# Kernel optimization log

Hardware: AMD Instinct MI355X
Metric: run time of the kernel (lower is better)

Reference implementation:

```python
import jax, jax.numpy as jnp
import numpy as np

NEG_INF = -1e30  # mask value used by QANet's apply_mask


def setup_inputs() -> dict:
    key = jax.random.key(0)
    ks = jax.random.split(key, 6)
    B, C, Q, H = 64, 1024, 128, 512
    return {
        "x_context": jax.random.normal(ks[0], (B, C, H), dtype=jnp.float32),
        "x_query": jax.random.normal(ks[1], (B, Q, H), dtype=jnp.float32),
        "context_mask": jnp.ones((B, C), dtype=jnp.float32),
        "query_mask": jnp.ones((B, Q), dtype=jnp.float32),
        "W0": jax.random.normal(ks[2], (H,), dtype=jnp.float32) * 0.05,
        "W1": jax.random.normal(ks[3], (H,), dtype=jnp.float32) * 0.05,
        "W2": jax.random.normal(ks[4], (H,), dtype=jnp.float32) * 0.05,
        "bias": jnp.zeros((1,), dtype=jnp.float32),
    }


def reference(x_context, x_query, context_mask, query_mask, W0, W1, W2, bias):
    # Trilinear similarity S[b,c,q] = q.W0 + c.W1 + (q*W2).c + bias
    # (original computes [B,Q,C] then transposes; we build [B,C,Q] directly)
    sub0 = jnp.einsum('bqh,h->bq', x_query, W0)          # [B,Q]
    sub1 = jnp.einsum('bch,h->bc', x_context, W1)        # [B,C]
    sub2 = jnp.einsum('bch,bqh->bcq', x_context, x_query * W2)  # [B,C,Q]
    S = sub2 + sub1[:, :, None] + sub0[:, None, :] + bias  # [B,C,Q]

    mq = query_mask[:, None, :]    # [B,1,Q]
    mc = context_mask[:, :, None]  # [B,C,1]

    # context-to-query: softmax over query axis, masked by query_mask
    S_ = jax.nn.softmax(S + (1.0 - mq) * NEG_INF, axis=-1)  # [B,C,Q]
    c2q = jnp.einsum('bcq,bqh->bch', S_, x_query)           # [B,C,H]

    # query-to-context: softmax over context axis, masked by context_mask
    S_c = jax.nn.softmax(S + (1.0 - mc) * NEG_INF, axis=1)  # [B,C,Q]
    S_T = jnp.swapaxes(S_c, 1, 2)                            # [B,Q,C]
    # (S_ @ S_T) @ x_context, associated as S_ @ (S_T @ x_context)
    tmp = jnp.einsum('bqc,bch->bqh', S_T, x_context)        # [B,Q,H]
    q2c = jnp.einsum('bcq,bqh->bch', S_, tmp)               # [B,C,H]
    return c2q, q2c
```

## Files before the change

kernel.cpp:

```cpp
#include <hip/hip_runtime.h>

#define BB 64
#define CC 1024
#define QQ 128
#define HH 512

typedef short bf16x8 __attribute__((ext_vector_type(8)));
typedef float f32x4 __attribute__((ext_vector_type(4)));

#define GLD16(g, l)                                                            \
    __builtin_amdgcn_global_load_lds(                                          \
        (const __attribute__((address_space(1))) unsigned int*)(g),            \
        (__attribute__((address_space(3))) unsigned int*)(l), 16, 0, 0)

__device__ __forceinline__ unsigned short f2bf(float f) {
    unsigned u = __float_as_uint(f);
    u += 0x7FFF + ((u >> 16) & 1);
    return (unsigned short)(u >> 16);
}
__device__ __forceinline__ unsigned pk2(float lo, float hi) {
    return (unsigned)f2bf(lo) | ((unsigned)f2bf(hi) << 16);
}

__global__ __launch_bounds__(256) void k_sub0(const float* __restrict__ xq,
                                              const float* __restrict__ w0,
                                              float* __restrict__ sub0,
                                              float* __restrict__ colsum) {
    if (blockIdx.x < 32) colsum[blockIdx.x * 256 + threadIdx.x] = 0.0f;
    int wave = threadIdx.x >> 6;
    int lane = threadIdx.x & 63;
    int row  = blockIdx.x * 4 + wave;
    const float* p = xq + (size_t)row * HH + lane * 8;
    float4 a0 = *(const float4*)(p);
    float4 a1 = *(const float4*)(p + 4);
    float4 b0 = *(const float4*)(w0 + lane * 8);
    float4 b1 = *(const float4*)(w0 + lane * 8 + 4);
    float s = a0.x*b0.x + a0.y*b0.y + a0.z*b0.z + a0.w*b0.w
            + a1.x*b1.x + a1.y*b1.y + a1.z*b1.z + a1.w*b1.w;
    #pragma unroll
    for (int off = 32; off; off >>= 1) s += __shfl_xor(s, off);
    if (lane == 0) sub0[row] = s;
}

__global__ __launch_bounds__(256) void k_prep(const float* __restrict__ xq,
                                              const float* __restrict__ w2,
                                              const float* __restrict__ qmask,
                                              unsigned short* __restrict__ xqw2b,
                                              unsigned short* __restrict__ xqmT) {
    int b  = blockIdx.y;
    int ht = blockIdx.x * 128;
    int tid = threadIdx.x;
    __shared__ __align__(16) unsigned short sT[128][132];

    {
        int q  = tid >> 1;
        int hh = (tid & 1) * 64;
        float qm = qmask[b * QQ + q];
        const float* xp = xq + ((size_t)b * QQ + q) * HH + ht + hh;
        unsigned short* wr = xqw2b + ((size_t)b * QQ + q) * HH + ht + hh;
        #pragma unroll
        for (int i = 0; i < 16; i++) {
            float4 v = *(const float4*)(xp + i * 4);
            float4 w = *(const float4*)(w2 + ht + hh + i * 4);
            uint2 pw; pw.x = pk2(v.x * w.x, v.y * w.y);
                      pw.y = pk2(v.z * w.z, v.w * w.w);
            *(uint2*)(wr + i * 4) = pw;
            uint2 pm; pm.x = pk2(v.x * qm, v.y * qm);
                      pm.y = pk2(v.z * qm, v.w * qm);
            *(uint2*)(&sT[q][hh + i * 4]) = pm;
        }
    }
    __syncthreads();
    {
        int h  = tid >> 1;
        int qh = (tid & 1) * 64;
        unsigned short* orow = xqmT + ((size_t)b * HH + ht + h) * QQ + qh;
        #pragma unroll
        for (int i = 0; i < 8; i++) {
            uint4 o;
            o.x = (unsigned)sT[qh + i*8 + 0][h] | ((unsigned)sT[qh + i*8 + 1][h] << 16);
            o.y = (unsigned)sT[qh + i*8 + 2][h] | ((unsigned)sT[qh + i*8 + 3][h] << 16);
            o.z = (unsigned)sT[qh + i*8 + 4][h] | ((unsigned)sT[qh + i*8 + 5][h] << 16);
            o.w = (unsigned)sT[qh + i*8 + 6][h] | ((unsigned)sT[qh + i*8 + 7][h] << 16);
            *(uint4*)(orow + i * 8) = o;
        }
    }
}

__global__ __launch_bounds__(256) void k_scores(
    const float* __restrict__ xc, const unsigned short* __restrict__ xqw2b,
    const float* __restrict__ w1, const float* __restrict__ cmask,
    const float* __restrict__ qmask, const float* __restrict__ bias,
    const float* __restrict__ sub0, unsigned short* __restrict__ Ebf,
    float* __restrict__ rowsum, float* __restrict__ colsum) {
    int b  = blockIdx.y;
    int c0 = blockIdx.x * 64;
    int tid  = threadIdx.x;
    int lane = tid & 63, wave = tid >> 6;
    int quad = lane >> 4, lcol = lane & 15;
    int wrow = (wave >> 1) * 32, wcol = (wave & 1) * 64;

    __shared__ __align__(16) unsigned short sA[2][64][32];
    __shared__ __align__(16) unsigned short sB[2][128][32];
    __shared__ float sW1[512];
    __shared__ float sSub1[64];
    __shared__ float sS0[128], sQm[128], sCm[64];
    __shared__ float sRowP[2][64], sColP[2][128];

    sW1[tid] = w1[tid]; sW1[tid + 256] = w1[tid + 256];
    if (tid < 128) {
        sS0[tid] = sub0[b * QQ + tid] + bias[0];
        sQm[tid] = qmask[b * QQ + tid];
    }
    if (tid < 64) sCm[tid] = cmask[b * CC + c0 + tid];

    f32x4 acc[2][4];
    #pragma unroll
    for (int i = 0; i < 2; i++)
        #pragma unroll
        for (int j = 0; j < 4; j++) acc[i][j] = (f32x4)0.0f;
    float s1 = 0.0f;

    int arow = tid >> 2, akh = (tid & 3) * 8;
    const float* gbase = xc + ((size_t)(b * CC + c0 + arow)) * HH + akh;

    __syncthreads();

    {
        float4 v0 = *(const float4*)(gbase);
        float4 v1 = *(const float4*)(gbase + 4);
        const float* wp = sW1 + akh;
        s1 += v0.x*wp[0] + v0.y*wp[1] + v0.z*wp[2] + v0.w*wp[3]
            + v1.x*wp[4] + v1.y*wp[5] + v1.z*wp[6] + v1.w*wp[7];
        uint4 p;
        p.x = pk2(v0.x, v0.y); p.y = pk2(v0.z, v0.w);
        p.z = pk2(v1.x, v1.y); p.w = pk2(v1.z, v1.w);
        *(uint4*)&sA[0][arow][akh] = p;
    }
    #pragma unroll
    for (int j = 0; j < 2; j++) {
        int chunk = wave * 2 + j;
        int row = chunk * 16 + (lane >> 2);
        GLD16(xqw2b + ((size_t)b * QQ + row) * HH + (lane & 3) * 8,
              (unsigned short*)sB[0] + chunk * 512);
    }
    __syncthreads();

    for (int t = 0; t < 16; ++t) {
        int cur = t & 1, alt = cur ^ 1;
        bool pf = (t < 15);
        int kn = (t + 1) * 32;
        float4 v0, v1;
        if (pf) {
            const float* gp = gbase + kn;
            v0 = *(const float4*)(gp);
            v1 = *(const float4*)(gp + 4);
            #pragma unroll
            for (int j = 0; j < 2; j++) {
                int chunk = wave * 2 + j;
                int row = chunk * 16 + (lane >> 2);
                GLD16(xqw2b + ((size_t)b * QQ + row) * HH + kn + (lane & 3) * 8,
                      (unsigned short*)sB[alt] + chunk * 512);
            }
        }
        bf16x8 af[2];
        #pragma unroll
        for (int mi = 0; mi < 2; mi++)
            af[mi] = *(const bf16x8*)&sA[cur][wrow + mi * 16 + lcol][quad * 8];
        #pragma unroll
        for (int ni = 0; ni < 4; ni++) {
            bf16x8 bfr = *(const bf16x8*)&sB[cur][wcol + ni * 16 + lcol][quad * 8];
            #pragma unroll
            for (int mi = 0; mi < 2; mi++)
                acc[mi][ni] = __builtin_amdgcn_mfma_f32_16x16x32_bf16(
                    af[mi], bfr, acc[mi][ni], 0, 0, 0);
        }
        if (pf) {
            const float* wp = sW1 + kn + akh;
            s1 += v0.x*wp[0] + v0.y*wp[1] + v0.z*wp[2] + v0.w*wp[3]
                + v1.x*wp[4] + v1.y*wp[5] + v1.z*wp[6] + v1.w*wp[7];
            uint4 p;
            p.x = pk2(v0.x, v0.y); p.y = pk2(v0.z, v0.w);
            p.z = pk2(v1.x, v1.y); p.w = pk2(v1.z, v1.w);
            *(uint4*)&sA[alt][arow][akh] = p;
        }
        __syncthreads();
    }

    s1 += __shfl_xor(s1, 1);
    s1 += __shfl_xor(s1, 2);
    if ((tid & 3) == 0) sSub1[arow] = s1;
    __syncthreads();

    float rsp[2][4];
    float csp[4] = {0.f, 0.f, 0.f, 0.f};
    #pragma unroll
    for (int mi = 0; mi < 2; mi++)
        #pragma unroll
        for (int r = 0; r < 4; r++) rsp[mi][r] = 0.f;

    #pragma unroll
    for (int mi = 0; mi < 2; mi++) {
        #pragma unroll
        for (int ni = 0; ni < 4; ni++) {
            int col = wcol + ni * 16 + lcol;
            float qm = sQm[col], s0 = sS0[col];
            #pragma unroll
            for (int r = 0; r < 4; r++) {
                int row = wrow + mi * 16 + quad * 4 + r;
                float e = __expf(acc[mi][ni][r] + sSub1[row] + s0);
                acc[mi][ni][r] = e;
                rsp[mi][r] += e * qm;
                csp[ni] += e * sCm[row];
            }
        }
    }
    #pragma unroll
    for (int mi = 0; mi < 2; mi++)
        #pragma unroll
        for (int r = 0; r < 4; r++) {
            float v = rsp[mi][r];
            v += __shfl_xor(v, 1); v += __shfl_xor(v, 2);
            v += __shfl_xor(v, 4); v += __shfl_xor(v, 8);
            if (lcol == 0) sRowP[wave & 1][wrow + mi * 16 + quad * 4 + r] = v;
        }
    #pragma unroll
    for (int ni = 0; ni < 4; ni++) {
        float v = csp[ni];
        v += __shfl_xor(v, 16); v += __shfl_xor(v, 32);
        if (quad == 0) sColP[wave >> 1][wcol + ni * 16 + lcol] = v;
    }
    #pragma unroll
    for (int mi = 0; mi < 2; mi++)
        #pragma unroll
        for (int ni = 0; ni < 4; ni++) {
            int col = wcol + ni * 16 + lcol;
            #pragma unroll
            for (int r = 0; r < 4; r++) {
                int row = wrow + mi * 16 + quad * 4 + r;
                Ebf[((size_t)(b * CC + c0 + row)) * QQ + col] = f2bf(acc[mi][ni][r]);
            }
        }
    __syncthreads();
    if (tid < 64)
        rowsum[(size_t)b * CC + c0 + tid] = sRowP[0][tid] + sRowP[1][tid];
    if (tid < 128)
        atomicAdd(&colsum[b * QQ + tid], sColP[0][tid] + sColP[1][tid]);
}

__global__ __launch_bounds__(256) void k_tmp(
    const unsigned short* __restrict__ Ebf, const float* __restrict__ xc,
    const float* __restrict__ cmask, const float* __restrict__ qmask,
    const float* __restrict__ colsum, unsigned short* __restrict__ tmpT) {
    int b  = blockIdx.y;
    int h0 = (blockIdx.x >> 1) * 64;
    int q0 = (blockIdx.x & 1) * 64;
    int tid  = threadIdx.x;
    int lane = tid & 63, wave = tid >> 6;
    int quad = lane >> 4, lcol = lane & 15;
    int wrow = (wave >> 1) * 32;
    int wcol = (wave & 1) * 32;

    __shared__ __align__(16) unsigned int sAu[2][64 * 16];
    __shared__ __align__(16) unsigned int sBu[2][64 * 16];
    __shared__ float sInv[64];
    if (tid < 64) sInv[tid] = qmask[b * QQ + q0 + tid] / colsum[b * QQ + q0 + tid];

    f32x4 acc[2][2];
    #pragma unroll
    for (int i = 0; i < 2; i++) { acc[i][0] = (f32x4)0.f; acc[i][1] = (f32x4)0.f; }

    int tp = tid >> 4;
    int tq = tid & 15;

    const unsigned short* ebase = Ebf + ((size_t)b * CC + 2 * tp) * QQ + q0 + tq * 4;
    const float*          xbase = xc  + ((size_t)b * CC + 2 * tp) * HH + h0 + tq * 4;
    const float*          mbase = cmask + (size_t)b * CC + 2 * tp;

    {
        union { uint2 v; unsigned short s[4]; } r0, r1;
        r0.v = *(const uint2*)(ebase);
        r1.v = *(const uint2*)(ebase + QQ);
        float cm0 = mbase[0];
        float cm1 = mbase[1];
        float4 f0 = *(const float4*)(xbase);
        float4 f1 = *(const float4*)(xbase + HH);
        #pragma unroll
        for (int j = 0; j < 4; j++) {
            int q = tq * 4 + j;
            unsigned pk = (unsigned)r0.s[j] | ((unsigned)r1.s[j] << 16);
            sAu[0][q * 16 + (((tp >> 2) ^ (q >> 3 & 3)) << 2) + (tp & 3)] = pk;
        }
        float a0[4] = {f0.x, f0.y, f0.z, f0.w};
        float a1[4] = {f1.x, f1.y, f1.z, f1.w};
        #pragma unroll
        for (int j = 0; j < 4; j++) {
            int h = tq * 4 + j;
            unsigned pk = pk2(a0[j] * cm0, a1[j] * cm1);
            sBu[0][h * 16 + (((tp >> 2) ^ (h >> 3 & 3)) << 2) + (tp & 3)] = pk;
        }
    }
    __syncthreads();

    for (int t = 0; t < 32; ++t) {
        int cur = t & 1, alt = cur ^ 1;
        bool pf = (t < 31);
        int cn = (t + 1) * 32;
        union { uint2 v; unsigned short s[4]; } r0, r1;
        float4 f0, f1;
        float cm0, cm1;
        if (pf) {
            r0.v = *(const uint2*)(ebase + (size_t)cn * QQ);
            r1.v = *(const uint2*)(ebase + (size_t)cn * QQ + QQ);
            cm0 = mbase[cn];
            cm1 = mbase[cn + 1];
            f0 = *(const float4*)(xbase + (size_t)cn * HH);
            f1 = *(const float4*)(xbase + (size_t)cn * HH + HH);
        }
        bf16x8 af[2];
        #pragma unroll
        for (int mi = 0; mi < 2; mi++) {
            int m = wrow + mi * 16 + lcol;
            af[mi] = *(const bf16x8*)(sAu[cur] + m * 16 + ((quad ^ (m >> 3 & 3)) << 2));
        }
        #pragma unroll
        for (int ni = 0; ni < 2; ni++) {
            int n = wcol + ni * 16 + lcol;
            bf16x8 bfr = *(const bf16x8*)(sBu[cur] + n * 16 + ((quad ^ (n >> 3 & 3)) << 2));
            #pragma unroll
            for (int mi = 0; mi < 2; mi++)
                acc[mi][ni] = __builtin_amdgcn_mfma_f32_16x16x32_bf16(
                    af[mi], bfr, acc[mi][ni], 0, 0, 0);
        }
        if (pf) {
            #pragma unroll
            for (int j = 0; j < 4; j++) {
                int q = tq * 4 + j;
                unsigned pk = (unsigned)r0.s[j] | ((unsigned)r1.s[j] << 16);
                sAu[alt][q * 16 + (((tp >> 2) ^ (q >> 3 & 3)) << 2) + (tp & 3)] = pk;
            }
            float a0[4] = {f0.x, f0.y, f0.z, f0.w};
            float a1[4] = {f1.x, f1.y, f1.z, f1.w};
            #pragma unroll
            for (int j = 0; j < 4; j++) {
                int h = tq * 4 + j;
                unsigned pk = pk2(a0[j] * cm0, a1[j] * cm1);
                sBu[alt][h * 16 + (((tp >> 2) ^ (h >> 3 & 3)) << 2) + (tp & 3)] = pk;
            }
        }
        __syncthreads();
    }
    #pragma unroll
    for (int mi = 0; mi < 2; mi++) {
        int qb = wrow + mi * 16 + quad * 4;
        #pragma unroll
        for (int ni = 0; ni < 2; ni++) {
            int h = wcol + ni * 16 + lcol;
            uint2 o;
            o.x = pk2(acc[mi][ni][0] * sInv[qb + 0], acc[mi][ni][1] * sInv[qb + 1]);
            o.y = pk2(acc[mi][ni][2] * sInv[qb + 2], acc[mi][ni][3] * sInv[qb + 3]);
            *(uint2*)(tmpT + ((size_t)b * HH + h0 + h) * QQ + q0 + qb) = o;
        }
    }
}

__global__ __launch_bounds__(256) void k_out(
    const unsigned short* __restrict__ Ebf, const unsigned short* __restrict__ xqmT,
    const unsigned short* __restrict__ tmpT, const float* __restrict__ rowsum,
    float* __restrict__ c2q, float* __restrict__ q2c) {
    int b  = blockIdx.z;
    int c0 = blockIdx.y * 128;
    int which = blockIdx.x & 1;
    int h0 = (blockIdx.x >> 1) * 128;
    const unsigned short* Bsrc = which ? tmpT : xqmT;
    float* dst = which ? q2c : c2q;
    int tid  = threadIdx.x;
    int lane = tid & 63, wave = tid >> 6;
    int quad = lane >> 4, lcol = lane & 15;
    int wrow = (wave >> 1) * 64, wcol = (wave & 1) * 64;

    __shared__ __align__(16) unsigned short sA[2][128][32];
    __shared__ __align__(16) unsigned short sB[2][128][32];
    __shared__ float sInvR[128];
    if (tid < 128) sInvR[tid] = 1.0f / rowsum[(size_t)b * CC + c0 + tid];

    f32x4 acc[4][4];
    #pragma unroll
    for (int i = 0; i < 4; i++)
        #pragma unroll
        for (int j = 0; j < 4; j++) acc[i][j] = (f32x4)0.f;

    #pragma unroll
    for (int j = 0; j < 2; j++) {
        int chunk = wave * 2 + j;
        int row = chunk * 16 + (lane >> 2);
        int kb  = (lane & 3) * 8;
        GLD16(Ebf  + ((size_t)b * CC + c0 + row) * QQ + kb,
              (unsigned short*)sA[0] + chunk * 512);
        GLD16(Bsrc + ((size_t)b * HH + h0 + row) * QQ + kb,
              (unsigned short*)sB[0] + chunk * 512);
    }
    __syncthreads();

    for (int t = 0; t < 4; ++t) {
        int cur = t & 1, alt = cur ^ 1;
        bool pf = (t < 3);
        int kn = (t + 1) * 32;
        if (pf) {
            #pragma unroll
            for (int j = 0; j < 2; j++) {
                int chunk = wave * 2 + j;
                int row = chunk * 16 + (lane >> 2);
                int kb  = (lane & 3) * 8;
                GLD16(Ebf  + ((size_t)b * CC + c0 + row) * QQ + kn + kb,
                      (unsigned short*)sA[alt] + chunk * 512);
                GLD16(Bsrc + ((size_t)b * HH + h0 + row) * QQ + kn + kb,
                      (unsigned short*)sB[alt] + chunk * 512);
            }
        }
        bf16x8 af[4];
        #pragma unroll
        for (int mi = 0; mi < 4; mi++)
            af[mi] = *(const bf16x8*)&sA[cur][wrow + mi * 16 + lcol][quad * 8];
        #pragma unroll
        for (int ni = 0; ni < 4; ni++) {
            bf16x8 bfr = *(const bf16x8*)&sB[cur][wcol + ni * 16 + lcol][quad * 8];
            #pragma unroll
            for (int mi = 0; mi < 4; mi++)
                acc[mi][ni] = __builtin_amdgcn_mfma_f32_16x16x32_bf16(
                    af[mi], bfr, acc[mi][ni], 0, 0, 0);
        }
        __syncthreads();
    }
    #pragma unroll
    for (int mi = 0; mi < 4; mi++) {
        int rb = wrow + mi * 16 + quad * 4;
        float ir0 = sInvR[rb], ir1 = sInvR[rb + 1], ir2 = sInvR[rb + 2], ir3 = sInvR[rb + 3];
        #pragma unroll
        for (int ni = 0; ni < 4; ni++) {
            int col = h0 + wcol + ni * 16 + lcol;
            size_t o0 = ((size_t)b * CC + c0 + rb) * HH + col;
            dst[o0]          = acc[mi][ni][0] * ir0;
            dst[o0 + HH]     = acc[mi][ni][1] * ir1;
            dst[o0 + 2*HH]   = acc[mi][ni][2] * ir2;
            dst[o0 + 3*HH]   = acc[mi][ni][3] * ir3;
        }
    }
}

extern "C" void kernel_launch(void* const* d_in, const int* in_sizes, int n_in,
                              void* d_out, int out_size, void* d_ws, size_t ws_size,
                              hipStream_t stream) {
    const float* xc    = (const float*)d_in[0];
    const float* xq    = (const float*)d_in[1];
    const float* cmask = (const float*)d_in[2];
    const float* qmask = (const float*)d_in[3];
    const float* w0    = (const float*)d_in[4];
    const float* w1    = (const float*)d_in[5];
    const float* w2    = (const float*)d_in[6];
    const float* bias  = (const float*)d_in[7];

    float* out = (float*)d_out;
    float* c2q = out;
    float* q2c = out + (size_t)BB * CC * HH;

    unsigned short* Ebf   = (unsigned short*)d_ws;
    unsigned short* xqw2b = Ebf   + (size_t)BB * CC * QQ;
    unsigned short* xqmT  = xqw2b + (size_t)BB * QQ * HH;
    unsigned short* tmpT  = xqmT  + (size_t)BB * QQ * HH;
    float* rowsum = (float*)(tmpT + (size_t)BB * QQ * HH);
    float* colsum = rowsum + (size_t)BB * CC;
    float* sub0   = colsum + (size_t)BB * QQ;

    k_sub0  <<<dim3(BB * QQ / 4),          256, 0, stream>>>(xq, w0, sub0, colsum);
    k_prep  <<<dim3(HH / 128, BB),         256, 0, stream>>>(xq, w2, qmask, xqw2b, xqmT);
    k_scores<<<dim3(CC / 64, BB),          256, 0, stream>>>(xc, xqw2b, w1, cmask, qmask,
                                                             bias, sub0, Ebf, rowsum, colsum);
    k_tmp   <<<dim3((HH / 64) * 2, BB),    256, 0, stream>>>(Ebf, xc, cmask, qmask,
                                                             colsum, tmpT);
    k_out   <<<dim3((HH / 128) * 2, CC / 128, BB), 256, 0, stream>>>(Ebf, xqmT, tmpT,
                                                                     rowsum, c2q, q2c);
}
```

Before: 491.0 us.

## Swizzle block IDs across XCDs and widen k_tmp tile to full Q

Result: faster. 458.1 us (-6.7%).

```diff
diff --git a/kernel.cpp b/kernel.cpp
--- a/kernel.cpp
+++ b/kernel.cpp
@@ -20,6 +20,10 @@
 }
 __device__ __forceinline__ unsigned pk2(float lo, float hi) {
     return (unsigned)f2bf(lo) | ((unsigned)f2bf(hi) << 16);
+}
+
+__device__ __forceinline__ unsigned xcd_swz(unsigned orig, unsigned nwg) {
+    return (orig & 7u) * (nwg >> 3) + (orig >> 3);
 }
 
 __global__ __launch_bounds__(256) void k_sub0(const float* __restrict__ xq,
@@ -93,8 +97,9 @@
     const float* __restrict__ qmask, const float* __restrict__ bias,
     const float* __restrict__ sub0, unsigned short* __restrict__ Ebf,
     float* __restrict__ rowsum, float* __restrict__ colsum) {
-    int b  = blockIdx.y;
-    int c0 = blockIdx.x * 64;
+    unsigned swz = xcd_swz(blockIdx.x, CC / 64 * BB);
+    int b  = swz >> 4;
+    int c0 = (swz & 15) * 64;
     int tid  = threadIdx.x;
     int lane = tid & 63, wave = tid >> 6;
     int quad = lane >> 4, lcol = lane & 15;
@@ -252,42 +257,42 @@
     const unsigned short* __restrict__ Ebf, const float* __restrict__ xc,
     const float* __restrict__ cmask, const float* __restrict__ qmask,
     const float* __restrict__ colsum, unsigned short* __restrict__ tmpT) {
-    int b  = blockIdx.y;
-    int h0 = (blockIdx.x >> 1) * 64;
-    int q0 = (blockIdx.x & 1) * 64;
+    unsigned swz = xcd_swz(blockIdx.x, HH / 64 * BB);
+    int b  = swz >> 3;
+    int h0 = (swz & 7) * 64;
     int tid  = threadIdx.x;
     int lane = tid & 63, wave = tid >> 6;
     int quad = lane >> 4, lcol = lane & 15;
-    int wrow = (wave >> 1) * 32;
+    int wrow = (wave >> 1) * 64;
     int wcol = (wave & 1) * 32;
 
-    __shared__ __align__(16) unsigned int sAu[2][64 * 16];
+    __shared__ __align__(16) unsigned int sAu[2][128 * 16];
     __shared__ __align__(16) unsigned int sBu[2][64 * 16];
-    __shared__ float sInv[64];
-    if (tid < 64) sInv[tid] = qmask[b * QQ + q0 + tid] / colsum[b * QQ + q0 + tid];
-
-    f32x4 acc[2][2];
-    #pragma unroll
-    for (int i = 0; i < 2; i++) { acc[i][0] = (f32x4)0.f; acc[i][1] = (f32x4)0.f; }
+    __shared__ float sInv[128];
+    if (tid < 128) sInv[tid] = qmask[b * QQ + tid] / colsum[b * QQ + tid];
+
+    f32x4 acc[4][2];
+    #pragma unroll
+    for (int i = 0; i < 4; i++) { acc[i][0] = (f32x4)0.f; acc[i][1] = (f32x4)0.f; }
 
     int tp = tid >> 4;
     int tq = tid & 15;
 
-    const unsigned short* ebase = Ebf + ((size_t)b * CC + 2 * tp) * QQ + q0 + tq * 4;
+    const unsigned short* ebase = Ebf + ((size_t)b * CC + 2 * tp) * QQ + tq * 8;
     const float*          xbase = xc  + ((size_t)b * CC + 2 * tp) * HH + h0 + tq * 4;
     const float*          mbase = cmask + (size_t)b * CC + 2 * tp;
 
     {
-        union { uint2 v; unsigned short s[4]; } r0, r1;
-        r0.v = *(const uint2*)(ebase);
-        r1.v = *(const uint2*)(ebase + QQ);
+        union { uint4 v; unsigned short s[8]; } r0, r1;
+        r0.v = *(const uint4*)(ebase);
+        r1.v = *(const uint4*)(ebase + QQ);
         float cm0 = mbase[0];
         float cm1 = mbase[1];
         float4 f0 = *(const float4*)(xbase);
         float4 f1 = *(const float4*)(xbase + HH);
         #pragma unroll
-        for (int j = 0; j < 4; j++) {
-            int q = tq * 4 + j;
+        for (int j = 0; j < 8; j++) {
+            int q = tq * 8 + j;
             unsigned pk = (unsigned)r0.s[j] | ((unsigned)r1.s[j] << 16);
             sAu[0][q * 16 + (((tp >> 2) ^ (q >> 3 & 3)) << 2) + (tp & 3)] = pk;
         }
@@ -306,20 +311,20 @@
         int cur = t & 1, alt = cur ^ 1;
         bool pf = (t < 31);
         int cn = (t + 1) * 32;
-        union { uint2 v; unsigned short s[4]; } r0, r1;
+        union { uint4 v; unsigned short s[8]; } r0, r1;
         float4 f0, f1;
         float cm0, cm1;
         if (pf) {
-            r0.v = *(const uint2*)(ebase + (size_t)cn * QQ);
-            r1.v = *(const uint2*)(ebase + (size_t)cn * QQ + QQ);
+            r0.v = *(const uint4*)(ebase + (size_t)cn * QQ);
+            r1.v = *(const uint4*)(ebase + (size_t)cn * QQ + QQ);
             cm0 = mbase[cn];
             cm1 = mbase[cn + 1];
             f0 = *(const float4*)(xbase + (size_t)cn * HH);
             f1 = *(const float4*)(xbase + (size_t)cn * HH + HH);
         }
-        bf16x8 af[2];
-        #pragma unroll
-        for (int mi = 0; mi < 2; mi++) {
+        bf16x8 af[4];
+        #pragma unroll
+        for (int mi = 0; mi < 4; mi++) {
             int m = wrow + mi * 16 + lcol;
             af[mi] = *(const bf16x8*)(sAu[cur] + m * 16 + ((quad ^ (m >> 3 & 3)) << 2));
         }
@@ -328,14 +333,14 @@
             int n = wcol + ni * 16 + lcol;
             bf16x8 bfr = *(const bf16x8*)(sBu[cur] + n * 16 + ((quad ^ (n >> 3 & 3)) << 2));
             #pragma unroll
-            for (int mi = 0; mi < 2; mi++)
+            for (int mi = 0; mi < 4; mi++)
                 acc[mi][ni] = __builtin_amdgcn_mfma_f32_16x16x32_bf16(
                     af[mi], bfr, acc[mi][ni], 0, 0, 0);
         }
         if (pf) {
             #pragma unroll
-            for (int j = 0; j < 4; j++) {
-                int q = tq * 4 + j;
+            for (int j = 0; j < 8; j++) {
+                int q = tq * 8 + j;
                 unsigned pk = (unsigned)r0.s[j] | ((unsigned)r1.s[j] << 16);
                 sAu[alt][q * 16 + (((tp >> 2) ^ (q >> 3 & 3)) << 2) + (tp & 3)] = pk;
             }
@@ -351,7 +356,7 @@
         __syncthreads();
     }
     #pragma unroll
-    for (int mi = 0; mi < 2; mi++) {
+    for (int mi = 0; mi < 4; mi++) {
         int qb = wrow + mi * 16 + quad * 4;
         #pragma unroll
         for (int ni = 0; ni < 2; ni++) {
@@ -359,7 +364,7 @@
             uint2 o;
             o.x = pk2(acc[mi][ni][0] * sInv[qb + 0], acc[mi][ni][1] * sInv[qb + 1]);
             o.y = pk2(acc[mi][ni][2] * sInv[qb + 2], acc[mi][ni][3] * sInv[qb + 3]);
-            *(uint2*)(tmpT + ((size_t)b * HH + h0 + h) * QQ + q0 + qb) = o;
+            *(uint2*)(tmpT + ((size_t)b * HH + h0 + h) * QQ + qb) = o;
         }
     }
 }
@@ -368,10 +373,12 @@
     const unsigned short* __restrict__ Ebf, const unsigned short* __restrict__ xqmT,
     const unsigned short* __restrict__ tmpT, const float* __restrict__ rowsum,
     float* __restrict__ c2q, float* __restrict__ q2c) {
-    int b  = blockIdx.z;
-    int c0 = blockIdx.y * 128;
-    int which = blockIdx.x & 1;
-    int h0 = (blockIdx.x >> 1) * 128;
+    unsigned swz = xcd_swz(blockIdx.x, (HH / 128) * 2 * (CC / 128) * BB);
+    int x  = swz & 7;
+    int c0 = ((swz >> 3) & 7) * 128;
+    int b  = swz >> 6;
+    int which = x & 1;
+    int h0 = (x >> 1) * 128;
     const unsigned short* Bsrc = which ? tmpT : xqmT;
     float* dst = which ? q2c : c2q;
     int tid  = threadIdx.x;
@@ -472,12 +479,12 @@
     float* colsum = rowsum + (size_t)BB * CC;
     float* sub0   = colsum + (size_t)BB * QQ;
 
-    k_sub0  <<<dim3(BB * QQ / 4),          256, 0, stream>>>(xq, w0, sub0, colsum);
-    k_prep  <<<dim3(HH / 128, BB),         256, 0, stream>>>(xq, w2, qmask, xqw2b, xqmT);
-    k_scores<<<dim3(CC / 64, BB),          256, 0, stream>>>(xc, xqw2b, w1, cmask, qmask,
-                                                             bias, sub0, Ebf, rowsum, colsum);
-    k_tmp   <<<dim3((HH / 64) * 2, BB),    256, 0, stream>>>(Ebf, xc, cmask, qmask,
-                                                             colsum, tmpT);
-    k_out   <<<dim3((HH / 128) * 2, CC / 128, BB), 256, 0, stream>>>(Ebf, xqmT, tmpT,
-                                                                     rowsum, c2q, q2c);
-}
+    k_sub0  <<<dim3(BB * QQ / 4),                 256, 0, stream>>>(xq, w0, sub0, colsum);
+    k_prep  <<<dim3(HH / 128, BB),                256, 0, stream>>>(xq, w2, qmask, xqw2b, xqmT);
+    k_scores<<<dim3(CC / 64 * BB),                256, 0, stream>>>(xc, xqw2b, w1, cmask, qmask,
+                                                                    bias, sub0, Ebf, rowsum, colsum);
+    k_tmp   <<<dim3(HH / 64 * BB),                256, 0, stream>>>(Ebf, xc, cmask, qmask,
+                                                                    colsum, tmpT);
+    k_out   <<<dim3((HH / 128) * 2 * (CC / 128) * BB), 256, 0, stream>>>(Ebf, xqmT, tmpT,
+                                                                          rowsum, c2q, q2c);
+}
```
